# Kernel optimization log

Measured on AMD Instinct MI355X. Metric: run time of the kernel, lower is better.

## Reference

```python
import jax, jax.numpy as jnp
import numpy as np

HEADS = 8
DIM_HEAD = 64
EPS = 1e-5


def _layernorm(x, g, b):
    m = jnp.mean(x, axis=-1, keepdims=True)
    v = jnp.mean((x - m) ** 2, axis=-1, keepdims=True)
    return (x - m) * jax.lax.rsqrt(v + EPS) * g + b


def setup_inputs() -> dict:
    key = jax.random.key(0)
    ks = jax.random.split(key, 8)
    b, c, hh, ww = 4, 256, 48, 48
    inner = HEADS * DIM_HEAD  # 512
    s = 0.02
    return {
        "x": jax.random.normal(ks[0], (b, c, hh, ww), jnp.float32),
        "Wq": jax.random.normal(ks[1], (c, inner), jnp.float32) * s,
        "Wk": jax.random.normal(ks[2], (c, inner), jnp.float32) * s,
        "Wv": jax.random.normal(ks[3], (c, inner), jnp.float32) * s,
        "Wo": jax.random.normal(ks[4], (inner, c), jnp.float32) * s,
        "bo": jnp.zeros((c,), jnp.float32),
        "g1": jnp.ones((c,), jnp.float32),
        "b1": jnp.zeros((c,), jnp.float32),
        "g2": jnp.ones((c,), jnp.float32),
        "b2": jnp.zeros((c,), jnp.float32),
        "Wf1": jax.random.normal(ks[5], (c, 2 * c), jnp.float32) * s,
        "bf1": jnp.zeros((2 * c,), jnp.float32),
        "Wf2": jax.random.normal(ks[6], (2 * c, c), jnp.float32) * s,
        "bf2": jnp.zeros((c,), jnp.float32),
        "Wp": jax.random.normal(ks[7], (c, c), jnp.float32) * s,
        "bp": jnp.zeros((c,), jnp.float32),
    }


def reference(x, Wq, Wk, Wv, Wo, bo, g1, b1, g2, b2, Wf1, bf1, Wf2, bf2, Wp, bp):
    b, c, hh, ww = x.shape
    n = hh * ww
    scale = DIM_HEAD ** -0.5
    x_in = x
    t = jnp.transpose(x.reshape(b, c, n), (0, 2, 1))  # [b, n, c]

    # --- CrossAttention (self-attn, context=None) ---
    tn = _layernorm(t, g1, b1)
    q = (tn @ Wq).reshape(b, n, HEADS, DIM_HEAD)
    k = (tn @ Wk).reshape(b, n, HEADS, DIM_HEAD)
    v = (tn @ Wv).reshape(b, n, HEADS, DIM_HEAD)
    sim = jnp.einsum("bihd,bjhd->bhij", q, k) * scale  # [b,h,n,n]
    attn = jax.nn.softmax(sim, axis=-1)
    o = jnp.einsum("bhij,bjhd->bihd", attn, v).reshape(b, n, HEADS * DIM_HEAD)
    t = o @ Wo + bo + t

    # --- FeedForward: Linear -> GELU(exact) -> Linear ---
    f = jax.nn.gelu(_layernorm(t, g2, b2) @ Wf1 + bf1, approximate=False)
    t = f @ Wf2 + bf2 + t

    # back to image and 1x1 conv (Wp[c_in, c_out])
    xi = jnp.transpose(t, (0, 2, 1)).reshape(b, c, hh, ww)
    y = jnp.einsum("bchw,co->bohw", xi, Wp) + bp[None, :, None, None]
    return y + x_in
```

## Files before the change

### kernel.cpp

```cpp
#include <hip/hip_runtime.h>
#include <math.h>

#define B_    4
#define C_    256
#define N_    2304
#define H_    8
#define DH_   64
#define IN_   512
#define ROWS_ 9216
#define NHALF 1152

typedef __attribute__((ext_vector_type(8))) short short8;
typedef __attribute__((ext_vector_type(4))) float f32x4;
typedef __attribute__((ext_vector_type(16))) float f32x16;

__device__ __forceinline__ unsigned short f2bf(float f) {
    unsigned int u = __float_as_uint(f);
    u += 0x7fffu + ((u >> 16) & 1u);
    return (unsigned short)(u >> 16);
}

__device__ __forceinline__ float bf2f(unsigned short u) {
    return __uint_as_float(((unsigned)u) << 16);
}

__device__ __forceinline__ float fexp2(float x) {
    return __builtin_amdgcn_exp2f(x);
}

__device__ __forceinline__ float gelu_fast(float x) {
    float x2 = x * x;
    float u  = x * fmaf(0.044715f, x2, 1.0f);
    float e  = fexp2(-2.3022082f * u);
    return x * __builtin_amdgcn_rcpf(1.0f + e);
}

__device__ __forceinline__ unsigned cvtpk(float lo, float hi) {
    unsigned r;
    asm("v_cvt_pk_bf16_f32 %0, %1, %2" : "=v"(r) : "v"(lo), "v"(hi));
    return r;
}

__device__ __forceinline__ void gload_lds16(const void* g, void* l) {
    __builtin_amdgcn_global_load_lds(
        (const __attribute__((address_space(1))) unsigned int*)g,
        (__attribute__((address_space(3))) unsigned int*)l, 16, 0, 0);
}

__device__ __forceinline__ const short8* frg(const short* base, int row, int chunk) {
    return (const short8*)(base + (row << 6) + (((chunk) ^ (row & 7)) << 3));
}

__device__ __forceinline__ int swz2(int row) {
    return (row & 7) ^ ((row >> 3) & 3);
}
__device__ __forceinline__ const short8* frg2(const short* base, int row, int chunk) {
    return (const short8*)(base + (row << 6) + (((chunk) ^ swz2(row)) << 3));
}

__global__ __launch_bounds__(256)
void k_pre(const float* __restrict__ Wq, const float* __restrict__ Wk,
           const float* __restrict__ Wv, const float* __restrict__ Wo,
           const float* __restrict__ Wf1, const float* __restrict__ Wf2,
           const float* __restrict__ Wp,
           unsigned short* Wqh, unsigned short* Wkh, unsigned short* Wvh,
           unsigned short* Woh, unsigned short* Wf1h, unsigned short* Wf2h,
           unsigned short* Wph,
           const float* __restrict__ x, float* __restrict__ T,
           unsigned short* __restrict__ TNh,
           const float* __restrict__ g1, const float* __restrict__ b1) {
    __shared__ float tile[32][257];
    int bid = blockIdx.x;
    int tid = threadIdx.x;
    if (bid < 1792) {
        int wz = bid >> 8;
        int rem = bid & 255;
        int nBase = (rem & 15) * 32;
        int kBase = (rem >> 4) * 32;
        const float* src; unsigned short* dst; int K, N;
        switch (wz) {
            case 0: src = Wq;  dst = Wqh;  K = 256; N = 512; break;
            case 1: src = Wk;  dst = Wkh;  K = 256; N = 512; break;
            case 2: src = Wv;  dst = Wvh;  K = 256; N = 512; break;
            case 3: src = Wo;  dst = Woh;  K = 512; N = 256; break;
            case 4: src = Wf1; dst = Wf1h; K = 256; N = 512; break;
            case 5: src = Wf2; dst = Wf2h; K = 512; N = 256; break;
            default: src = Wp; dst = Wph;  K = 256; N = 256; break;
        }
        if (nBase >= N || kBase >= K) return;
        float scl = (wz == 0) ? 0.18033688f : 1.0f;
        int tx = tid & 31, ty = tid >> 5;
        #pragma unroll
        for (int i = 0; i < 32; i += 8)
            tile[ty + i][tx] = src[(size_t)(kBase + ty + i) * N + nBase + tx];
        __syncthreads();
        #pragma unroll
        for (int i = 0; i < 32; i += 8)
            dst[(size_t)(nBase + ty + i) * K + kBase + tx] = f2bf(tile[tx][ty + i] * scl);
    } else {
        int idx = bid - 1792;
        int bb = idx / 72;
        int nBase = (idx - bb * 72) * 32;
        int tx = tid & 31;
        int tg = tid >> 5;
        const float* xp = x + (size_t)bb * C_ * N_ + nBase + tx;
        #pragma unroll
        for (int i = 0; i < 32; ++i) {
            int c = tg * 32 + i;
            tile[tx][c] = xp[(size_t)c * N_];
        }
        __syncthreads();
        int w = tid >> 6, lane = tid & 63;
        float g0 = g1[lane], ga = g1[lane + 64], gb2 = g1[lane + 128], gc = g1[lane + 192];
        float b0 = b1[lane], ba = b1[lane + 64], bb2 = b1[lane + 128], bc = b1[lane + 192];
        #pragma unroll
        for (int r8 = 0; r8 < 8; ++r8) {
            int row = w * 8 + r8;
            float v0 = tile[row][lane],       v1 = tile[row][lane + 64];
            float v2 = tile[row][lane + 128], v3 = tile[row][lane + 192];
            float s = v0 + v1 + v2 + v3;
            #pragma unroll
            for (int m = 1; m < 64; m <<= 1) s += __shfl_xor(s, m);
            float mean = s * (1.0f / C_);
            float d0 = v0 - mean, d1 = v1 - mean, d2 = v2 - mean, d3 = v3 - mean;
            float s2 = d0 * d0 + d1 * d1 + d2 * d2 + d3 * d3;
            #pragma unroll
            for (int m = 1; m < 64; m <<= 1) s2 += __shfl_xor(s2, m);
            float rs = rsqrtf(s2 * (1.0f / C_) + 1e-5f);
            size_t o = (size_t)(bb * N_ + nBase + row) * C_ + lane;
            T[o]       = v0; T[o + 64]  = v1; T[o + 128] = v2; T[o + 192] = v3;
            TNh[o]       = f2bf(d0 * rs * g0 + b0);
            TNh[o + 64]  = f2bf(d1 * rs * ga + ba);
            TNh[o + 128] = f2bf(d2 * rs * gb2 + bb2);
            TNh[o + 192] = f2bf(d3 * rs * gc + bc);
        }
    }
}

__global__ __launch_bounds__(256)
void k_layernorm_bf16(const float* __restrict__ in, unsigned short* __restrict__ out,
                      const float* __restrict__ g, const float* __restrict__ b) {
    int wv = threadIdx.x >> 6;
    int lane = threadIdx.x & 63;
    int row = blockIdx.x * 4 + wv;
    float4 v = ((const float4*)(in + (size_t)row * C_))[lane];
    float s = v.x + v.y + v.z + v.w;
    #pragma unroll
    for (int m = 1; m < 64; m <<= 1) s += __shfl_xor(s, m);
    float mean = s * (1.0f / C_);
    float dx = v.x - mean, dy = v.y - mean, dz = v.z - mean, dw = v.w - mean;
    float s2 = dx * dx + dy * dy + dz * dz + dw * dw;
    #pragma unroll
    for (int m = 1; m < 64; m <<= 1) s2 += __shfl_xor(s2, m);
    float rs = rsqrtf(s2 * (1.0f / C_) + 1e-5f);
    float4 gv = ((const float4*)g)[lane];
    float4 bv = ((const float4*)b)[lane];
    ushort4 o;
    o.x = f2bf(dx * rs * gv.x + bv.x);
    o.y = f2bf(dy * rs * gv.y + bv.y);
    o.z = f2bf(dz * rs * gv.z + bv.z);
    o.w = f2bf(dw * rs * gv.w + bv.w);
    *(ushort4*)(out + (size_t)row * C_ + lane * 4) = o;
}

template <int EP>
__global__ __launch_bounds__(256)
void k_gemm64(const short* __restrict__ A, const short* __restrict__ Bt,
              void* __restrict__ Out, const float* __restrict__ bias,
              const float* __restrict__ Res, int M, int N, int K) {
    __shared__ __align__(16) short As[64 * 64];
    __shared__ __align__(16) short Bs[64 * 64];
    int tid = threadIdx.x;
    int w = tid >> 6;
    int lane = tid & 63;
    int l15 = lane & 15;
    int lg = lane >> 4;
    int wr = w >> 1, wc = w & 1;
    int rowBase = blockIdx.y * 64;
    int colBase = blockIdx.x * 64;

    f32x4 acc[2][2];
    #pragma unroll
    for (int m = 0; m < 2; ++m)
        #pragma unroll
        for (int n = 0; n < 2; ++n) acc[m][n] = (f32x4){0.f, 0.f, 0.f, 0.f};

    for (int k0 = 0; k0 < K; k0 += 64) {
        __syncthreads();
        #pragma unroll
        for (int a = 0; a < 2; ++a) {
            int rr = (w << 4) + (a << 3) + (lane >> 3);
            int cc = (lane & 7) ^ (lane >> 3);
            gload_lds16(A + (size_t)(rowBase + rr) * K + k0 + cc * 8,
                        As + (((w << 4) + (a << 3)) << 6));
            gload_lds16(Bt + (size_t)(colBase + rr) * K + k0 + cc * 8,
                        Bs + (((w << 4) + (a << 3)) << 6));
        }
        asm volatile("s_waitcnt vmcnt(0)" ::: "memory");
        __syncthreads();
        short8 af[2][2], bf[2][2];
        #pragma unroll
        for (int m = 0; m < 2; ++m) {
            af[m][0] = *frg(As, wr * 32 + m * 16 + l15, lg);
            af[m][1] = *frg(As, wr * 32 + m * 16 + l15, 4 + lg);
        }
        #pragma unroll
        for (int n = 0; n < 2; ++n) {
            bf[n][0] = *frg(Bs, wc * 32 + n * 16 + l15, lg);
            bf[n][1] = *frg(Bs, wc * 32 + n * 16 + l15, 4 + lg);
        }
        #pragma unroll
        for (int m = 0; m < 2; ++m)
            #pragma unroll
            for (int n = 0; n < 2; ++n) {
                acc[m][n] = __builtin_amdgcn_mfma_f32_16x16x32_bf16(af[m][0], bf[n][0], acc[m][n], 0, 0, 0);
                acc[m][n] = __builtin_amdgcn_mfma_f32_16x16x32_bf16(af[m][1], bf[n][1], acc[m][n], 0, 0, 0);
            }
    }

    int arB = rowBase + wr * 32;
    int brB = colBase + wc * 32;
    int bb = 0;
    if (EP == 5) bb = brB / N_;
    #pragma unroll
    for (int m = 0; m < 2; ++m) {
        #pragma unroll
        for (int i = 0; i < 4; ++i) {
            int ar = arB + m * 16 + lg * 4 + i;
            #pragma unroll
            for (int n = 0; n < 2; ++n) {
                int br = brB + n * 16 + l15;
                float v = acc[m][n][i];
                if constexpr (EP == 2) {
                    size_t o = (size_t)ar * N + br;
                    ((float*)Out)[o] = v + bias[br] + Res[o];
                } else if constexpr (EP == 3) {
                    ((unsigned short*)Out)[(size_t)ar * N + br] = f2bf(gelu_fast(v + bias[br]));
                } else if constexpr (EP == 4) {
                    size_t o = (size_t)ar * N + br;
                    ((unsigned short*)Out)[o] = f2bf(v + bias[br] + Res[o]);
                } else {
                    size_t o = ((size_t)(bb * C_) + ar) * N_ + (br - bb * N_);
                    ((float*)Out)[o] = v + bias[ar] + Res[o];
                }
            }
        }
    }
}

__global__ __launch_bounds__(256)
void k_gemm_qkv(const short* __restrict__ TNh, const short* __restrict__ Wqh,
                const short* __restrict__ Wkh, const short* __restrict__ Wvh,
                unsigned short* __restrict__ Qb, unsigned short* __restrict__ Kb,
                unsigned short* __restrict__ Vt) {
    __shared__ __align__(16) short As[64 * 64];
    __shared__ __align__(16) short Bs[64 * 64];
    int bid = blockIdx.x;
    int z = bid / 1152;
    int rem = bid - z * 1152;
    int tid = threadIdx.x;
    int w = tid >> 6;
    int lane = tid & 63;
    int l15 = lane & 15;
    int lg = lane >> 4;
    int wr = w >> 1, wc = w & 1;
    const short *A, *Bt;
    int rowBase, colBase;
    if (z < 2) {
        A = TNh; Bt = z ? Wkh : Wqh;
        colBase = (rem & 7) * 64;
        rowBase = (rem >> 3) * 64;
    } else {
        A = Wvh; Bt = TNh;
        colBase = (rem % 144) * 64;
        rowBase = (rem / 144) * 64;
    }
    const int K = C_;

    f32x4 acc[2][2];
    #pragma unroll
    for (int m = 0; m < 2; ++m)
        #pragma unroll
        for (int n = 0; n < 2; ++n) acc[m][n] = (f32x4){0.f, 0.f, 0.f, 0.f};

    for (int k0 = 0; k0 < K; k0 += 64) {
        __syncthreads();
        #pragma unroll
        for (int a = 0; a < 2; ++a) {
            int rr = (w << 4) + (a << 3) + (lane >> 3);
            int cc = (lane & 7) ^ (lane >> 3);
            gload_lds16(A + (size_t)(rowBase + rr) * K + k0 + cc * 8,
                        As + (((w << 4) + (a << 3)) << 6));
            gload_lds16(Bt + (size_t)(colBase + rr) * K + k0 + cc * 8,
                        Bs + (((w << 4) + (a << 3)) << 6));
        }
        asm volatile("s_waitcnt vmcnt(0)" ::: "memory");
        __syncthreads();
        short8 af[2][2], bf[2][2];
        #pragma unroll
        for (int m = 0; m < 2; ++m) {
            af[m][0] = *frg(As, wr * 32 + m * 16 + l15, lg);
            af[m][1] = *frg(As, wr * 32 + m * 16 + l15, 4 + lg);
        }
        #pragma unroll
        for (int n = 0; n < 2; ++n) {
            bf[n][0] = *frg(Bs, wc * 32 + n * 16 + l15, lg);
            bf[n][1] = *frg(Bs, wc * 32 + n * 16 + l15, 4 + lg);
        }
        #pragma unroll
        for (int m = 0; m < 2; ++m)
            #pragma unroll
            for (int n = 0; n < 2; ++n) {
                acc[m][n] = __builtin_amdgcn_mfma_f32_16x16x32_bf16(af[m][0], bf[n][0], acc[m][n], 0, 0, 0);
                acc[m][n] = __builtin_amdgcn_mfma_f32_16x16x32_bf16(af[m][1], bf[n][1], acc[m][n], 0, 0, 0);
            }
    }

    int arB = rowBase + wr * 32;
    int brB = colBase + wc * 32;
    if (z < 2) {
        unsigned short* Out = z ? Kb : Qb;
        #pragma unroll
        for (int m = 0; m < 2; ++m)
            #pragma unroll
            for (int i = 0; i < 4; ++i) {
                int ar = arB + m * 16 + lg * 4 + i;
                #pragma unroll
                for (int n = 0; n < 2; ++n)
                    Out[(size_t)ar * IN_ + brB + n * 16 + l15] = f2bf(acc[m][n][i]);
            }
    } else {
        int bb = brB / N_;
        #pragma unroll
        for (int m = 0; m < 2; ++m)
            #pragma unroll
            for (int i = 0; i < 4; ++i) {
                int ar = arB + m * 16 + lg * 4 + i;
                #pragma unroll
                for (int n = 0; n < 2; ++n) {
                    int br = brB + n * 16 + l15;
                    Vt[((size_t)(bb * IN_) + ar) * N_ + (br - bb * N_)] = f2bf(acc[m][n][i]);
                }
            }
    }
}

__global__ __launch_bounds__(256, 3)
void k_flash_mfma(const short* __restrict__ Qb, const short* __restrict__ Kb,
                  const short* __restrict__ Vt,
                  unsigned short* O0, unsigned short* O1,
                  float* __restrict__ Lsum) {
    __shared__ __align__(16) short Ks[2][64 * 64];
    __shared__ __align__(16) short Vs[2][64 * 64];
    int tid = threadIdx.x;
    int lane = tid & 63;
    int l31 = lane & 31;
    int h5 = lane >> 5;
    int w = tid >> 6;

    int logical = (blockIdx.x & 7) * 144 + (blockIdx.x >> 3);
    int pair = logical / 18;
    int qi = logical - pair * 18;
    int bh = pair & 31;
    int half = pair >> 5;
    int bb = bh >> 3, h = bh & 7;
    int qBase = qi * 128;
    int h0 = half * NHALF;

    const short* Qp = Qb + ((size_t)bb * N_ + qBase + w * 32) * IN_ + h * DH_;
    const short* Kp = Kb + (size_t)bb * N_ * IN_ + h * DH_;
    const short* Vp = Vt + ((size_t)bb * IN_ + h * DH_) * N_;

    short8 qf[4];
    #pragma unroll
    for (int kk = 0; kk < 4; ++kk)
        qf[kk] = *(const short8*)(Qp + (size_t)l31 * IN_ + kk * 16 + h5 * 8);

    short8 ones;
    #pragma unroll
    for (int j = 0; j < 8; ++j) ones[j] = (short)0x3F80;

    auto STAGE = [&](int buf, int kt2) {
        #pragma unroll
        for (int j = 0; j < 2; ++j) {
            int br = (w << 4) + (j << 3);
            int rr = br + (lane >> 3);
            int cc = (lane & 7) ^ (lane >> 3) ^ ((2 * w + j) & 3);
            gload_lds16(Kp + (size_t)(kt2 + rr) * IN_ + cc * 8, &Ks[buf][br << 6]);
            gload_lds16(Vp + (size_t)rr * N_ + kt2 + cc * 8, &Vs[buf][br << 6]);
        }
    };

    f32x16 oacc0 = (f32x16)(0.0f);
    f32x16 oacc1 = (f32x16)(0.0f);
    f32x16 lacc  = (f32x16)(0.0f);

    STAGE(0, h0);
    const int NT = NHALF / 64;
    for (int t = 0; t < NT; ++t) {
        asm volatile("s_waitcnt vmcnt(0)" ::: "memory");
        __builtin_amdgcn_s_barrier();
        __builtin_amdgcn_sched_barrier(0);
        if (t + 1 < NT) STAGE((t + 1) & 1, h0 + (t + 1) * 64);
        const short* Kc = Ks[t & 1];
        const short* Vc = Vs[t & 1];

        short8 pa[4];
        #pragma unroll
        for (int s = 0; s < 2; ++s) {
            f32x16 stv = (f32x16)(0.0f);
            __builtin_amdgcn_s_setprio(1);
            #pragma unroll
            for (int kk = 0; kk < 4; ++kk) {
                short8 kf = *frg2(Kc, s * 32 + l31, kk * 2 + h5);
                stv = __builtin_amdgcn_mfma_f32_32x32x16_bf16(kf, qf[kk], stv, 0, 0, 0);
            }
            __builtin_amdgcn_s_setprio(0);
            unsigned u[8];
            #pragma unroll
            for (int q = 0; q < 4; ++q) {
                u[2 * q]     = cvtpk(fexp2(stv[4 * q + 0]), fexp2(stv[4 * q + 1]));
                u[2 * q + 1] = cvtpk(fexp2(stv[4 * q + 2]), fexp2(stv[4 * q + 3]));
            }
            asm volatile("v_permlane32_swap_b32 %0, %1" : "+v"(u[0]), "+v"(u[2]));
            asm volatile("v_permlane32_swap_b32 %0, %1" : "+v"(u[1]), "+v"(u[3]));
            asm volatile("v_permlane32_swap_b32 %0, %1" : "+v"(u[4]), "+v"(u[6]));
            asm volatile("v_permlane32_swap_b32 %0, %1" : "+v"(u[5]), "+v"(u[7]));
            union { unsigned uu[4]; short8 s8; } c0, c1;
            c0.uu[0] = u[0]; c0.uu[1] = u[1]; c0.uu[2] = u[2]; c0.uu[3] = u[3];
            c1.uu[0] = u[4]; c1.uu[1] = u[5]; c1.uu[2] = u[6]; c1.uu[3] = u[7];
            pa[2 * s]     = c0.s8;
            pa[2 * s + 1] = c1.s8;
        }

        __builtin_amdgcn_s_setprio(1);
        #pragma unroll
        for (int kk = 0; kk < 4; ++kk) {
            short8 vf0 = *frg2(Vc, l31, kk * 2 + h5);
            short8 vf1 = *frg2(Vc, 32 + l31, kk * 2 + h5);
            lacc  = __builtin_amdgcn_mfma_f32_32x32x16_bf16(pa[kk], ones, lacc, 0, 0, 0);
            oacc0 = __builtin_amdgcn_mfma_f32_32x32x16_bf16(pa[kk], vf0, oacc0, 0, 0, 0);
            oacc1 = __builtin_amdgcn_mfma_f32_32x32x16_bf16(pa[kk], vf1, oacc1, 0, 0, 0);
        }
        __builtin_amdgcn_s_setprio(0);
    }

    unsigned short* OpH = (half == 0) ? O0 : O1;
    unsigned short* Op = OpH + ((size_t)bb * N_ + qBase + w * 32) * IN_ + h * DH_;
    #pragma unroll
    for (int reg = 0; reg < 16; ++reg) {
        int q = (reg & 3) + 8 * (reg >> 2) + 4 * h5;
        Op[(size_t)q * IN_ + l31]      = f2bf(oacc0[reg]);
        Op[(size_t)q * IN_ + 32 + l31] = f2bf(oacc1[reg]);
    }
    if (l31 == 0) {
        float* Lp = Lsum + (((size_t)half * B_ + bb) * H_ + h) * N_ + qBase + w * 32;
        #pragma unroll
        for (int reg = 0; reg < 16; ++reg) {
            int q = (reg & 3) + 8 * (reg >> 2) + 4 * h5;
            Lp[q] = lacc[reg];
        }
    }
}

__global__ __launch_bounds__(256)
void k_combine(const unsigned short* p0, const unsigned short* p1,
               const float* __restrict__ Lsum, unsigned short* Ob) {
    int wv = threadIdx.x >> 6;
    int lane = threadIdx.x & 63;
    int row = blockIdx.x * 4 + wv;
    int bb = row / N_;
    int n = row - bb * N_;
    int hh = lane >> 3;
    float l0 = Lsum[(((size_t)0 * B_ + bb) * H_ + hh) * N_ + n];
    float l1 = Lsum[(((size_t)1 * B_ + bb) * H_ + hh) * N_ + n];
    float inv = 1.0f / (l0 + l1);
    size_t off = (size_t)row * IN_ + lane * 8;
    short8 a0 = *(const short8*)(p0 + off);
    short8 a1 = *(const short8*)(p1 + off);
    unsigned short o[8];
    #pragma unroll
    for (int j = 0; j < 8; ++j)
        o[j] = f2bf((bf2f((unsigned short)a0[j]) + bf2f((unsigned short)a1[j])) * inv);
    *(uint4*)(Ob + off) = *(uint4*)o;
}

extern "C" void kernel_launch(void* const* d_in, const int* in_sizes, int n_in,
                              void* d_out, int out_size, void* d_ws, size_t ws_size,
                              hipStream_t stream) {
    (void)in_sizes; (void)n_in; (void)out_size; (void)ws_size;
    const float* x   = (const float*)d_in[0];
    const float* Wq  = (const float*)d_in[1];
    const float* Wk  = (const float*)d_in[2];
    const float* Wv  = (const float*)d_in[3];
    const float* Wo  = (const float*)d_in[4];
    const float* bo  = (const float*)d_in[5];
    const float* g1  = (const float*)d_in[6];
    const float* b1  = (const float*)d_in[7];
    const float* g2  = (const float*)d_in[8];
    const float* b2  = (const float*)d_in[9];
    const float* Wf1 = (const float*)d_in[10];
    const float* bf1 = (const float*)d_in[11];
    const float* Wf2 = (const float*)d_in[12];
    const float* bf2 = (const float*)d_in[13];
    const float* Wp  = (const float*)d_in[14];
    const float* bp  = (const float*)d_in[15];
    float* out = (float*)d_out;
    float* ws  = (float*)d_ws;

    float* T    = ws;
    float* T2   = ws + 2359296;
    unsigned short* TNh = (unsigned short*)(ws + 4718592);
    short* Qb   = (short*)(ws + 5898240);
    short* Kb   = (short*)(ws + 8257536);
    short* Vt   = (short*)(ws + 10616832);
    unsigned short* Obh = (unsigned short*)(ws + 12976128);
    short* F    = (short*)(ws + 15335424);
    short* T3h  = (short*)(ws + 17694720);
    unsigned short* Wqh  = (unsigned short*)(ws + 18874368);
    unsigned short* Wkh  = (unsigned short*)(ws + 18939904);
    unsigned short* Wvh  = (unsigned short*)(ws + 19005440);
    unsigned short* Woh  = (unsigned short*)(ws + 19070976);
    unsigned short* Wf1h = (unsigned short*)(ws + 19136512);
    unsigned short* Wf2h = (unsigned short*)(ws + 19202048);
    unsigned short* Wph  = (unsigned short*)(ws + 19267584);
    unsigned short* Op0  = (unsigned short*)(ws + 19398656);
    unsigned short* Op1  = Obh;
    float* Lsum = ws + 24117248;

    k_pre<<<dim3(2080), 256, 0, stream>>>(Wq, Wk, Wv, Wo, Wf1, Wf2, Wp,
                                          Wqh, Wkh, Wvh, Woh, Wf1h, Wf2h, Wph,
                                          x, T, TNh, g1, b1);
    k_gemm_qkv<<<dim3(3456), 256, 0, stream>>>((const short*)TNh, (const short*)Wqh,
                                               (const short*)Wkh, (const short*)Wvh,
                                               (unsigned short*)Qb, (unsigned short*)Kb,
                                               (unsigned short*)Vt);
    k_flash_mfma<<<dim3(1152), 256, 0, stream>>>(Qb, Kb, Vt, Op0, Op1, Lsum);
    k_combine<<<2304, 256, 0, stream>>>(Op0, Op1, Lsum, Obh);
    k_gemm64<2><<<dim3(4, 144), 256, 0, stream>>>((const short*)Obh, (const short*)Woh, T2, bo, T, ROWS_, C_, IN_);
    k_layernorm_bf16<<<2304, 256, 0, stream>>>(T2, TNh, g2, b2);
    k_gemm64<3><<<dim3(8, 144), 256, 0, stream>>>((const short*)TNh, (const short*)Wf1h, F, bf1, nullptr, ROWS_, IN_, C_);
    k_gemm64<4><<<dim3(4, 144), 256, 0, stream>>>((const short*)F, (const short*)Wf2h, T3h, bf2, T2, ROWS_, C_, IN_);
    k_gemm64<5><<<dim3(144, 4), 256, 0, stream>>>((const short*)Wph, (const short*)T3h, out, bp, x, C_, ROWS_, C_);
}
```

Baseline: 141.9 us.

## Process two 128-row query tiles per flash block to reuse staged K/V

Each flash-attention block now handles 256 query rows (two sets of 32 rows per wave) instead of 128, so every K/V tile staged into shared memory feeds twice as many MFMAs. The grid is halved to 576 blocks, the block-index remapping is adjusted to match, and launch bounds drop from 3 to 2 blocks per SM to leave room for the doubled accumulator registers. This cuts global-to-LDS traffic and barrier overhead per unit of work, but lowers occupancy and leaves fewer blocks to balance across CUs.

```diff
diff --git a/kernel.cpp b/kernel.cpp
--- a/kernel.cpp
+++ b/kernel.cpp
@@ -345,7 +345,7 @@
     }
 }
 
-__global__ __launch_bounds__(256, 3)
+__global__ __launch_bounds__(256, 2)
 void k_flash_mfma(const short* __restrict__ Qb, const short* __restrict__ Kb,
                   const short* __restrict__ Vt,
                   unsigned short* O0, unsigned short* O1,
@@ -358,23 +358,26 @@
     int h5 = lane >> 5;
     int w = tid >> 6;
 
-    int logical = (blockIdx.x & 7) * 144 + (blockIdx.x >> 3);
-    int pair = logical / 18;
-    int qi = logical - pair * 18;
+    int logical = (blockIdx.x & 7) * 72 + (blockIdx.x >> 3);
+    int pair = logical / 9;
+    int qi = logical - pair * 9;
     int bh = pair & 31;
     int half = pair >> 5;
     int bb = bh >> 3, h = bh & 7;
-    int qBase = qi * 128;
+    int qBase = qi * 256;
     int h0 = half * NHALF;
 
-    const short* Qp = Qb + ((size_t)bb * N_ + qBase + w * 32) * IN_ + h * DH_;
+    const short* QpA = Qb + ((size_t)bb * N_ + qBase + w * 32) * IN_ + h * DH_;
+    const short* QpB = QpA + (size_t)128 * IN_;
     const short* Kp = Kb + (size_t)bb * N_ * IN_ + h * DH_;
     const short* Vp = Vt + ((size_t)bb * IN_ + h * DH_) * N_;
 
-    short8 qf[4];
-    #pragma unroll
-    for (int kk = 0; kk < 4; ++kk)
-        qf[kk] = *(const short8*)(Qp + (size_t)l31 * IN_ + kk * 16 + h5 * 8);
+    short8 qfA[4], qfB[4];
+    #pragma unroll
+    for (int kk = 0; kk < 4; ++kk) {
+        qfA[kk] = *(const short8*)(QpA + (size_t)l31 * IN_ + kk * 16 + h5 * 8);
+        qfB[kk] = *(const short8*)(QpB + (size_t)l31 * IN_ + kk * 16 + h5 * 8);
+    }
 
     short8 ones;
     #pragma unroll
@@ -391,9 +394,26 @@
         }
     };
 
-    f32x16 oacc0 = (f32x16)(0.0f);
-    f32x16 oacc1 = (f32x16)(0.0f);
-    f32x16 lacc  = (f32x16)(0.0f);
+    auto SMPACK = [&](const f32x16& stv, short8& paLo, short8& paHi) {
+        unsigned u[8];
+        #pragma unroll
+        for (int q = 0; q < 4; ++q) {
+            u[2 * q]     = cvtpk(fexp2(stv[4 * q + 0]), fexp2(stv[4 * q + 1]));
+            u[2 * q + 1] = cvtpk(fexp2(stv[4 * q + 2]), fexp2(stv[4 * q + 3]));
+        }
+        asm volatile("v_permlane32_swap_b32 %0, %1" : "+v"(u[0]), "+v"(u[2]));
+        asm volatile("v_permlane32_swap_b32 %0, %1" : "+v"(u[1]), "+v"(u[3]));
+        asm volatile("v_permlane32_swap_b32 %0, %1" : "+v"(u[4]), "+v"(u[6]));
+        asm volatile("v_permlane32_swap_b32 %0, %1" : "+v"(u[5]), "+v"(u[7]));
+        union { unsigned uu[4]; short8 s8; } c0, c1;
+        c0.uu[0] = u[0]; c0.uu[1] = u[1]; c0.uu[2] = u[2]; c0.uu[3] = u[3];
+        c1.uu[0] = u[4]; c1.uu[1] = u[5]; c1.uu[2] = u[6]; c1.uu[3] = u[7];
+        paLo = c0.s8;
+        paHi = c1.s8;
+    };
+
+    f32x16 oaccA0 = (f32x16)(0.0f), oaccA1 = (f32x16)(0.0f), laccA = (f32x16)(0.0f);
+    f32x16 oaccB0 = (f32x16)(0.0f), oaccB1 = (f32x16)(0.0f), laccB = (f32x16)(0.0f);
 
     STAGE(0, h0);
     const int NT = NHALF / 64;
@@ -405,60 +425,63 @@
         const short* Kc = Ks[t & 1];
         const short* Vc = Vs[t & 1];
 
-        short8 pa[4];
-        #pragma unroll
-        for (int s = 0; s < 2; ++s) {
-            f32x16 stv = (f32x16)(0.0f);
-            __builtin_amdgcn_s_setprio(1);
-            #pragma unroll
-            for (int kk = 0; kk < 4; ++kk) {
-                short8 kf = *frg2(Kc, s * 32 + l31, kk * 2 + h5);
-                stv = __builtin_amdgcn_mfma_f32_32x32x16_bf16(kf, qf[kk], stv, 0, 0, 0);
-            }
-            __builtin_amdgcn_s_setprio(0);
-            unsigned u[8];
-            #pragma unroll
-            for (int q = 0; q < 4; ++q) {
-                u[2 * q]     = cvtpk(fexp2(stv[4 * q + 0]), fexp2(stv[4 * q + 1]));
-                u[2 * q + 1] = cvtpk(fexp2(stv[4 * q + 2]), fexp2(stv[4 * q + 3]));
-            }
-            asm volatile("v_permlane32_swap_b32 %0, %1" : "+v"(u[0]), "+v"(u[2]));
-            asm volatile("v_permlane32_swap_b32 %0, %1" : "+v"(u[1]), "+v"(u[3]));
-            asm volatile("v_permlane32_swap_b32 %0, %1" : "+v"(u[4]), "+v"(u[6]));
-            asm volatile("v_permlane32_swap_b32 %0, %1" : "+v"(u[5]), "+v"(u[7]));
-            union { unsigned uu[4]; short8 s8; } c0, c1;
-            c0.uu[0] = u[0]; c0.uu[1] = u[1]; c0.uu[2] = u[2]; c0.uu[3] = u[3];
-            c1.uu[0] = u[4]; c1.uu[1] = u[5]; c1.uu[2] = u[6]; c1.uu[3] = u[7];
-            pa[2 * s]     = c0.s8;
-            pa[2 * s + 1] = c1.s8;
-        }
-
+        f32x16 stvA0 = (f32x16)(0.0f), stvB0 = (f32x16)(0.0f);
+        f32x16 stvA1 = (f32x16)(0.0f), stvB1 = (f32x16)(0.0f);
         __builtin_amdgcn_s_setprio(1);
         #pragma unroll
         for (int kk = 0; kk < 4; ++kk) {
-            short8 vf0 = *frg2(Vc, l31, kk * 2 + h5);
-            short8 vf1 = *frg2(Vc, 32 + l31, kk * 2 + h5);
-            lacc  = __builtin_amdgcn_mfma_f32_32x32x16_bf16(pa[kk], ones, lacc, 0, 0, 0);
-            oacc0 = __builtin_amdgcn_mfma_f32_32x32x16_bf16(pa[kk], vf0, oacc0, 0, 0, 0);
-            oacc1 = __builtin_amdgcn_mfma_f32_32x32x16_bf16(pa[kk], vf1, oacc1, 0, 0, 0);
+            short8 kf = *frg2(Kc, l31, kk * 2 + h5);
+            stvA0 = __builtin_amdgcn_mfma_f32_32x32x16_bf16(kf, qfA[kk], stvA0, 0, 0, 0);
+            stvB0 = __builtin_amdgcn_mfma_f32_32x32x16_bf16(kf, qfB[kk], stvB0, 0, 0, 0);
+        }
+        #pragma unroll
+        for (int kk = 0; kk < 4; ++kk) {
+            short8 kf = *frg2(Kc, 32 + l31, kk * 2 + h5);
+            stvA1 = __builtin_amdgcn_mfma_f32_32x32x16_bf16(kf, qfA[kk], stvA1, 0, 0, 0);
+            stvB1 = __builtin_amdgcn_mfma_f32_32x32x16_bf16(kf, qfB[kk], stvB1, 0, 0, 0);
         }
         __builtin_amdgcn_s_setprio(0);
+
+        short8 paA[4], paB[4];
+        SMPACK(stvA0, paA[0], paA[1]);
+        SMPACK(stvB0, paB[0], paB[1]);
+        SMPACK(stvA1, paA[2], paA[3]);
+        SMPACK(stvB1, paB[2], paB[3]);
+
+        __builtin_amdgcn_s_setprio(1);
+        #pragma unroll
+        for (int kk = 0; kk < 4; ++kk) {
+            short8 vf = *frg2(Vc, l31, kk * 2 + h5);
+            short8 vg = *frg2(Vc, 32 + l31, kk * 2 + h5);
+            laccA  = __builtin_amdgcn_mfma_f32_32x32x16_bf16(paA[kk], ones, laccA, 0, 0, 0);
+            oaccA0 = __builtin_amdgcn_mfma_f32_32x32x16_bf16(paA[kk], vf, oaccA0, 0, 0, 0);
+            oaccA1 = __builtin_amdgcn_mfma_f32_32x32x16_bf16(paA[kk], vg, oaccA1, 0, 0, 0);
+            laccB  = __builtin_amdgcn_mfma_f32_32x32x16_bf16(paB[kk], ones, laccB, 0, 0, 0);
+            oaccB0 = __builtin_amdgcn_mfma_f32_32x32x16_bf16(paB[kk], vf, oaccB0, 0, 0, 0);
+            oaccB1 = __builtin_amdgcn_mfma_f32_32x32x16_bf16(paB[kk], vg, oaccB1, 0, 0, 0);
+        }
+        __builtin_amdgcn_s_setprio(0);
     }
 
     unsigned short* OpH = (half == 0) ? O0 : O1;
-    unsigned short* Op = OpH + ((size_t)bb * N_ + qBase + w * 32) * IN_ + h * DH_;
+    unsigned short* OpA = OpH + ((size_t)bb * N_ + qBase + w * 32) * IN_ + h * DH_;
+    unsigned short* OpB = OpA + (size_t)128 * IN_;
     #pragma unroll
     for (int reg = 0; reg < 16; ++reg) {
         int q = (reg & 3) + 8 * (reg >> 2) + 4 * h5;
-        Op[(size_t)q * IN_ + l31]      = f2bf(oacc0[reg]);
-        Op[(size_t)q * IN_ + 32 + l31] = f2bf(oacc1[reg]);
+        OpA[(size_t)q * IN_ + l31]      = f2bf(oaccA0[reg]);
+        OpA[(size_t)q * IN_ + 32 + l31] = f2bf(oaccA1[reg]);
+        OpB[(size_t)q * IN_ + l31]      = f2bf(oaccB0[reg]);
+        OpB[(size_t)q * IN_ + 32 + l31] = f2bf(oaccB1[reg]);
     }
     if (l31 == 0) {
-        float* Lp = Lsum + (((size_t)half * B_ + bb) * H_ + h) * N_ + qBase + w * 32;
+        float* LpA = Lsum + (((size_t)half * B_ + bb) * H_ + h) * N_ + qBase + w * 32;
+        float* LpB = LpA + 128;
         #pragma unroll
         for (int reg = 0; reg < 16; ++reg) {
             int q = (reg & 3) + 8 * (reg >> 2) + 4 * h5;
-            Lp[q] = lacc[reg];
+            LpA[q] = laccA[reg];
+            LpB[q] = laccB[reg];
         }
     }
 }
@@ -535,7 +558,7 @@
                                                (const short*)Wkh, (const short*)Wvh,
                                                (unsigned short*)Qb, (unsigned short*)Kb,
                                                (unsigned short*)Vt);
-    k_flash_mfma<<<dim3(1152), 256, 0, stream>>>(Qb, Kb, Vt, Op0, Op1, Lsum);
+    k_flash_mfma<<<dim3(576), 256, 0, stream>>>(Qb, Kb, Vt, Op0, Op1, Lsum);
     k_combine<<<2304, 256, 0, stream>>>(Op0, Op1, Lsum, Obh);
     k_gemm64<2><<<dim3(4, 144), 256, 0, stream>>>((const short*)Obh, (const short*)Woh, T2, bo, T, ROWS_, C_, IN_);
     k_layernorm_bf16<<<2304, 256, 0, stream>>>(T2, TNh, g2, b2);
```

Measured after the change: 147.8 us. 4.2% more time.
